# Kernel tuning notes

Hardware: AMD Instinct MI355X
Metric: run time of the kernel (lower is better)

## Reference

```python
import jax, jax.numpy as jnp
import numpy as np
from functools import partial

TOP_K = 2
LN_EPS = 1e-5


def setup_inputs() -> dict:
    key = jax.random.key(0)
    ks = jax.random.split(key, 4)
    B, T, H, F, E = 2, 2048, 1024, 4096, 8
    hidden_states = jax.random.normal(ks[0], (B, T, H), dtype=jnp.float32)
    # Router weights: original inits to zeros; use small random so routing is non-degenerate.
    router_w = jax.random.normal(ks[1], (E, H), dtype=jnp.float32) * 0.02
    router_b = jnp.zeros((E,), dtype=jnp.float32)
    W1 = jax.random.normal(ks[2], (E, H, F), dtype=jnp.float32) * (1.0 / np.sqrt(H))
    b1 = jnp.zeros((E, F), dtype=jnp.float32)
    W2 = jax.random.normal(ks[3], (E, F, H), dtype=jnp.float32) * (1.0 / np.sqrt(F))
    b2 = jnp.zeros((E, H), dtype=jnp.float32)
    ln_gamma = jnp.ones((H,), dtype=jnp.float32)
    ln_beta = jnp.zeros((H,), dtype=jnp.float32)
    return {"hidden_states": hidden_states, "router_w": router_w, "router_b": router_b,
            "W1": W1, "b1": b1, "W2": W2, "b2": b2,
            "ln_gamma": ln_gamma, "ln_beta": ln_beta}


def _layer_norm(x, gamma, beta):
    mu = jnp.mean(x, axis=-1, keepdims=True)
    var = jnp.var(x, axis=-1, keepdims=True)
    return (x - mu) * jax.lax.rsqrt(var + LN_EPS) * gamma + beta


def _moe_forward(hidden_states, router_w, router_b, W1, b1, W2, b2, ln_gamma, ln_beta):
    B, T, H = hidden_states.shape
    E = router_w.shape[0]
    N = B * T
    x = hidden_states.reshape(N, H)
    # Router (jitter=0.0, eval mode): logits [N, E]
    logits = x @ router_w.T + router_b
    topk_vals, topk_idx = jax.lax.top_k(logits, TOP_K)        # [N, K]
    topk_w = jax.nn.softmax(topk_vals, axis=-1)               # [N, K]
    # Scatter top-k weights into a dense combine matrix [N, E] (zeros elsewhere).
    probs = jnp.zeros((N, E), dtype=x.dtype).at[jnp.arange(N)[:, None], topk_idx].set(topk_w)
    # Per-expert FFN via scan over the (small, fixed) expert axis; each step is one
    # big GEMM over all tokens weighted by that expert's combine prob (0 for
    # tokens not routed to it) — same math as gather/MLP/scatter with no capacity drop.
    def body(acc, params_e):
        Wa, ba, Wb, bb, pe = params_e          # pe: [N]
        h = jax.nn.gelu(x @ Wa + ba, approximate=False)   # [N, F]
        y = h @ Wb + bb                                    # [N, H]
        return acc + y * pe[:, None], None
    out, _ = jax.lax.scan(body, jnp.zeros_like(x), (W1, b1, W2, b2, probs.T))
    out = out.reshape(B, T, H)
    return _layer_norm(out + hidden_states, ln_gamma, ln_beta)


def reference(hidden_states, router_w, router_b, W1, b1, W2, b2, ln_gamma, ln_beta):
    return _moe_forward(hidden_states, router_w, router_b, W1, b1, W2, b2, ln_gamma, ln_beta)
```

## Files before the change

kernel.cpp:

```cpp
#include <hip/hip_runtime.h>
#include <hip/hip_bf16.h>


typedef unsigned short u16;
typedef unsigned int u32;
typedef __attribute__((ext_vector_type(4))) float f32x4;
typedef __attribute__((ext_vector_type(8))) short s16x8;
typedef __attribute__((ext_vector_type(8))) unsigned short u16x8;

#define GLD16(gp, lp) __builtin_amdgcn_global_load_lds( \
    (const __attribute__((address_space(1))) void*)(gp), \
    (__attribute__((address_space(3))) void*)(lp), 16, 0, 0)

__device__ __forceinline__ u16 f2bf(float f) {
    union { float f; u32 u; } v; v.f = f;
    u32 u = v.u;
    return (u16)((u + 0x7fffu + ((u >> 16) & 1u)) >> 16);
}
__device__ __forceinline__ float bf2f(u16 h) {
    union { u32 u; float f; } v; v.u = ((u32)h) << 16; return v.f;
}

__device__ __forceinline__ float gelu_f(float v) {
    const float u = v * (0.7978845608f + 0.0356774081f * v * v);
    const float t = __expf(-2.0f * u);
    return v * __builtin_amdgcn_rcpf(1.0f + t);
}

__global__ void k_init(int* cc) { if (threadIdx.x < 16) cc[threadIdx.x] = 0; }

__device__ __forceinline__ void transp_nolds(
    const float* __restrict__ s, u16* __restrict__ d, int K, int N, int n0, int k0, int tid)
{
    const int n = n0 + tid;
    #pragma unroll 4
    for (int c8 = 0; c8 < 8; ++c8) {
        const int kb = k0 + c8 * 8;
        float v[8];
        #pragma unroll
        for (int j = 0; j < 8; ++j)
            v[j] = s[(size_t)(kb + j) * N + n];
        u16x8 o;
        #pragma unroll
        for (int j = 0; j < 8; ++j) o[j] = f2bf(v[j]);
        *(u16x8*)(d + (size_t)n * K + kb) = o;
    }
}

__global__ __launch_bounds__(256) void k_pre(
    const float* __restrict__ x, const float* __restrict__ rw, const float* __restrict__ rb,
    u16* __restrict__ xb, int* __restrict__ eidx, float* __restrict__ wgt, int* __restrict__ counts,
    const float* __restrict__ W1, u16* __restrict__ W1t)
{
    const int id = blockIdx.x;
    const int tid = threadIdx.x;

    if (id >= 1024) {
        const int id2 = id - 1024;
        const int e = id2 >> 8, rem = id2 & 255;
        const int nb = rem >> 4, kc = rem & 15;
        transp_nolds(W1 + (size_t)e * 1024 * 4096, W1t + (size_t)e * 1024 * 4096,
                     1024, 4096, nb * 256, kc * 64, tid);
        return;
    }

    const int wav = tid >> 6, lane = tid & 63;
    const int t = id * 4 + wav;
    const float* xt = x + (size_t)t * 1024;
    float acc[8] = {0.f,0.f,0.f,0.f,0.f,0.f,0.f,0.f};
    #pragma unroll
    for (int c = 0; c < 4; c++) {
        const int base = c * 256 + lane * 4;
        const float4 xv = *(const float4*)(xt + base);
        ushort4 pk;
        pk.x = f2bf(xv.x); pk.y = f2bf(xv.y); pk.z = f2bf(xv.z); pk.w = f2bf(xv.w);
        *(ushort4*)(xb + (size_t)t * 1024 + base) = pk;
        #pragma unroll
        for (int e = 0; e < 8; e++) {
            const float4 wv = *(const float4*)(rw + e * 1024 + base);
            acc[e] += xv.x * wv.x + xv.y * wv.y + xv.z * wv.z + xv.w * wv.w;
        }
    }
    #pragma unroll
    for (int e = 0; e < 8; e++) {
        #pragma unroll
        for (int s = 32; s; s >>= 1) acc[e] += __shfl_xor(acc[e], s);
    }
    if (lane == 0) {
        float v0 = -3e38f, v1 = -3e38f; int i0 = 0, i1 = 0;
        #pragma unroll
        for (int e = 0; e < 8; e++) {
            const float l = acc[e] + rb[e];
            if (l > v0) { v1 = v0; i1 = i0; v0 = l; i0 = e; }
            else if (l > v1) { v1 = l; i1 = e; }
        }
        const float w0 = 1.0f / (1.0f + expf(v1 - v0));
        eidx[2 * t] = i0; eidx[2 * t + 1] = i1;
        wgt[2 * t] = w0; wgt[2 * t + 1] = 1.0f - w0;
        atomicAdd(&counts[i0], 1); atomicAdd(&counts[i1], 1);
    }
}

__global__ __launch_bounds__(256) void k_place2(
    const int* __restrict__ eidx, const int* __restrict__ counts, int* __restrict__ cursors,
    int* __restrict__ offsets, int* __restrict__ rows, int* __restrict__ pos_of)
{
    int base[8];
    int s = 0;
    #pragma unroll
    for (int e = 0; e < 8; e++) { base[e] = s; s += counts[e]; }
    if (blockIdx.x == 0 && threadIdx.x == 0) {
        #pragma unroll
        for (int e = 0; e < 8; e++) offsets[e] = base[e];
        offsets[8] = s;
    }
    const int a = blockIdx.x * 256 + threadIdx.x;
    const int e = eidx[a];
    const int pos = base[e] + atomicAdd(&cursors[e], 1);
    rows[pos] = a >> 1;
    pos_of[a] = pos;
}

#define STAGE_T(b, k0) { \
    char* ad = (char*)At + (b) * 8192 + wav * 1024; \
    char* bd = (char*)Bt + (b) * 8192 + wav * 1024; \
    GLD16(a_src0 + (k0), ad); \
    GLD16(a_src1 + (k0), ad + 4096); \
    GLD16(b_src0 + (k0), bd); \
    GLD16(b_src1 + (k0), bd + 4096); }

#define COMPUTE_T(b) { \
    const u16* Abp = Ab + (b) * 4096; \
    const u16* Bbp = Bb + (b) * 4096; \
    s16x8 af[4], bfr[4]; \
    _Pragma("unroll") \
    for (int i = 0; i < 4; i++) { \
        af[i]  = *(const s16x8*)(Abp + i * 512); \
        bfr[i] = *(const s16x8*)(Bbp + i * 512); \
    } \
    __builtin_amdgcn_s_setprio(1); \
    _Pragma("unroll") \
    for (int mi = 0; mi < 4; mi++) \
        _Pragma("unroll") \
        for (int ni = 0; ni < 4; ni++) \
            acc[mi][ni] = __builtin_amdgcn_mfma_f32_16x16x32_bf16(af[mi], bfr[ni], acc[mi][ni], 0, 0, 0); \
    __builtin_amdgcn_s_setprio(0); }

#define VMCNT4 asm volatile("s_waitcnt vmcnt(4)" ::: "memory")
#define VMCNT0 asm volatile("s_waitcnt vmcnt(0)" ::: "memory")
#define BAR __builtin_amdgcn_s_barrier()

__global__ __launch_bounds__(256, 4) void k_gemm1f(
    const u16* __restrict__ xb, const u16* __restrict__ W1t, const float* __restrict__ b1,
    u16* __restrict__ hbuf, const int* __restrict__ rows, const int* __restrict__ offsets,
    const float* __restrict__ W2, u16* __restrict__ W2t)
{
    const int bid = blockIdx.x;
    const int tid = threadIdx.x;

    if (bid < 2048) {
        const int e = bid >> 8, rem = bid & 255;
        const int nb = rem >> 6, kc = rem & 63;
        transp_nolds(W2 + (size_t)e * 4096 * 1024, W2t + (size_t)e * 1024 * 4096,
                     4096, 1024, nb * 256, kc * 64, tid);
        return;
    }

    const int fid = bid - 2048;
    const int swz = (fid & 7) * 1024 + (fid >> 3);
    const int y = swz & 31, xx = (swz >> 5) & 31, e = swz >> 10;

    const int off = offsets[e], cnt = offsets[e + 1] - off;
    const int row0 = y * 128;
    if (row0 >= cnt) return;
    const int n0 = xx * 128;
    const int lane = tid & 63, wav = tid >> 6, lane15 = lane & 15;

    __shared__ u16 At[2][128][32];
    __shared__ u16 Bt[2][128][32];

    const int ar0 = tid >> 2;
    const int cl8 = (((tid & 3) ^ ((tid >> 3) & 3))) * 8;
    const int t0 = rows[off + min(row0 + ar0, cnt - 1)];
    const int t1 = rows[off + min(row0 + ar0 + 64, cnt - 1)];
    const u16* a_src0 = xb + (size_t)t0 * 1024 + cl8;
    const u16* a_src1 = xb + (size_t)t1 * 1024 + cl8;
    const u16* b_src0 = W1t + ((size_t)e * 4096 + n0 + ar0) * 1024 + cl8;
    const u16* b_src1 = b_src0 + (size_t)64 * 1024;

    f32x4 acc[4][4] = {};
    const int wr = wav >> 1, wc = wav & 1;
    const int koff = ((lane >> 4) ^ ((lane >> 1) & 3)) * 8;
    const u16* Ab = &At[0][wr * 64 + lane15][koff];
    const u16* Bb = &Bt[0][wc * 64 + lane15][koff];

    STAGE_T(0, 0);
    int b = 0;
    for (int k0 = 32; k0 < 1024; k0 += 32) {
        STAGE_T(b ^ 1, k0);
        VMCNT4;
        BAR;
        COMPUTE_T(b);
        BAR;
        b ^= 1;
    }
    VMCNT0;
    BAR;
    COMPUTE_T(b);

    const int rb4 = (lane >> 4) * 4;
    const int colbase = n0 + wc * 64 + lane15;
    float bias[4];
    #pragma unroll
    for (int ni = 0; ni < 4; ni++) bias[ni] = b1[e * 4096 + colbase + ni * 16];
    #pragma unroll
    for (int mi = 0; mi < 4; mi++) {
        #pragma unroll
        for (int j = 0; j < 4; j++) {
            const int lrow = wr * 64 + mi * 16 + rb4 + j;
            if (row0 + lrow < cnt) {
                const size_t gr = (size_t)(off + row0 + lrow);
                #pragma unroll
                for (int ni = 0; ni < 4; ni++) {
                    const float v = acc[mi][ni][j] + bias[ni];
                    hbuf[gr * 4096 + colbase + ni * 16] = f2bf(gelu_f(v));
                }
            }
        }
    }
}

__global__ __launch_bounds__(256, 4) void k_gemm2(
    const u16* __restrict__ hbuf, const u16* __restrict__ W2t, const float* __restrict__ b2,
    u16* __restrict__ yb, const int* __restrict__ offsets)
{
    const int fid = blockIdx.x;
    const int swz = (fid & 7) * 1024 + (fid >> 3);
    const int y = swz & 31, xx = (swz >> 5) & 7, z = swz >> 8;
    const int e = z >> 2, kq = z & 3;

    const int off = offsets[e], cnt = offsets[e + 1] - off;
    const int row0 = y * 128;
    if (row0 >= cnt) return;
    const int n0 = xx * 128;
    const int tid = threadIdx.x;
    const int lane = tid & 63, wav = tid >> 6, lane15 = lane & 15;
    const int kbase = kq * 1024;

    __shared__ u16 At[2][128][32];
    __shared__ u16 Bt[2][128][32];

    const int ar0 = tid >> 2;
    const int cl8 = (((tid & 3) ^ ((tid >> 3) & 3))) * 8;
    const u16* a_src0 = hbuf + (size_t)(off + min(row0 + ar0, cnt - 1)) * 4096 + kbase + cl8;
    const u16* a_src1 = hbuf + (size_t)(off + min(row0 + ar0 + 64, cnt - 1)) * 4096 + kbase + cl8;
    const u16* b_src0 = W2t + ((size_t)e * 1024 + n0 + ar0) * 4096 + kbase + cl8;
    const u16* b_src1 = b_src0 + (size_t)64 * 4096;

    f32x4 acc[4][4] = {};
    const int wr = wav >> 1, wc = wav & 1;
    const int koff = ((lane >> 4) ^ ((lane >> 1) & 3)) * 8;
    const u16* Ab = &At[0][wr * 64 + lane15][koff];
    const u16* Bb = &Bt[0][wc * 64 + lane15][koff];

    STAGE_T(0, 0);
    int b = 0;
    for (int k0 = 32; k0 < 1024; k0 += 32) {
        STAGE_T(b ^ 1, k0);
        VMCNT4;
        BAR;
        COMPUTE_T(b);
        BAR;
        b ^= 1;
    }
    VMCNT0;
    BAR;
    COMPUTE_T(b);

    u16* yy = yb + (size_t)kq * 8192 * 1024;
    const int rb4 = (lane >> 4) * 4;
    const int colbase = n0 + wc * 64 + lane15;
    float bias[4];
    #pragma unroll
    for (int ni = 0; ni < 4; ni++) bias[ni] = (kq == 0) ? b2[e * 1024 + colbase + ni * 16] : 0.f;
    #pragma unroll
    for (int mi = 0; mi < 4; mi++) {
        #pragma unroll
        for (int j = 0; j < 4; j++) {
            const int lrow = wr * 64 + mi * 16 + rb4 + j;
            if (row0 + lrow < cnt) {
                const size_t gr = (size_t)(off + row0 + lrow);
                #pragma unroll
                for (int ni = 0; ni < 4; ni++)
                    yy[gr * 1024 + colbase + ni * 16] = f2bf(acc[mi][ni][j] + bias[ni]);
            }
        }
    }
}

__global__ __launch_bounds__(256) void k_combine(
    const float* __restrict__ x, const u16* __restrict__ yb,
    const int* __restrict__ pos_of, const float* __restrict__ wgt,
    const float* __restrict__ gamma, const float* __restrict__ beta,
    float* __restrict__ out)
{
    const int t = blockIdx.x;
    const int tid = threadIdx.x;
    const int p0 = pos_of[2 * t], p1 = pos_of[2 * t + 1];
    const float w0 = wgt[2 * t], w1 = wgt[2 * t + 1];
    const int j4 = tid * 4;
    const float4 xv = *(const float4*)(x + (size_t)t * 1024 + j4);
    float s0[4] = {0.f, 0.f, 0.f, 0.f};
    float s1[4] = {0.f, 0.f, 0.f, 0.f};
    #pragma unroll
    for (int kq = 0; kq < 4; kq++) {
        const u16* ybq = yb + (size_t)kq * 8192 * 1024;
        const ushort4 u0 = *(const ushort4*)(ybq + (size_t)p0 * 1024 + j4);
        const ushort4 u1 = *(const ushort4*)(ybq + (size_t)p1 * 1024 + j4);
        s0[0] += bf2f(u0.x); s0[1] += bf2f(u0.y); s0[2] += bf2f(u0.z); s0[3] += bf2f(u0.w);
        s1[0] += bf2f(u1.x); s1[1] += bf2f(u1.y); s1[2] += bf2f(u1.z); s1[3] += bf2f(u1.w);
    }
    float a0 = xv.x + w0 * s0[0] + w1 * s1[0];
    float a1 = xv.y + w0 * s0[1] + w1 * s1[1];
    float a2 = xv.z + w0 * s0[2] + w1 * s1[2];
    float a3 = xv.w + w0 * s0[3] + w1 * s1[3];
    float s = a0 + a1 + a2 + a3;
    float q = a0 * a0 + a1 * a1 + a2 * a2 + a3 * a3;
    #pragma unroll
    for (int o = 32; o; o >>= 1) { s += __shfl_xor(s, o); q += __shfl_xor(q, o); }
    __shared__ float ls[4], lq[4];
    const int wav = tid >> 6, lane = tid & 63;
    if (lane == 0) { ls[wav] = s; lq[wav] = q; }
    __syncthreads();
    s = ls[0] + ls[1] + ls[2] + ls[3];
    q = lq[0] + lq[1] + lq[2] + lq[3];
    const float mu = s * (1.0f / 1024.0f);
    const float var = q * (1.0f / 1024.0f) - mu * mu;
    const float rs = rsqrtf(var + 1e-5f);
    const float4 g = *(const float4*)(gamma + j4);
    const float4 b = *(const float4*)(beta + j4);
    float4 o4;
    o4.x = (a0 - mu) * rs * g.x + b.x;
    o4.y = (a1 - mu) * rs * g.y + b.y;
    o4.z = (a2 - mu) * rs * g.z + b.z;
    o4.w = (a3 - mu) * rs * g.w + b.w;
    *(float4*)(out + (size_t)t * 1024 + j4) = o4;
}

extern "C" void kernel_launch(void* const* d_in, const int* in_sizes, int n_in,
                              void* d_out, int out_size, void* d_ws, size_t ws_size,
                              hipStream_t stream) {
    const float* x     = (const float*)d_in[0];
    const float* rw    = (const float*)d_in[1];
    const float* rb    = (const float*)d_in[2];
    const float* W1    = (const float*)d_in[3];
    const float* b1    = (const float*)d_in[4];
    const float* W2    = (const float*)d_in[5];
    const float* b2    = (const float*)d_in[6];
    const float* gamma = (const float*)d_in[7];
    const float* beta  = (const float*)d_in[8];
    float* out = (float*)d_out;

    char* p = (char*)d_ws;
    auto alloc = [&](size_t bytes) { char* r = p; p += (bytes + 255) & ~(size_t)255; return r; };
    int*   counts  = (int*)alloc(16 * sizeof(int));
    int*   cursors = counts + 8;
    int*   offsets = (int*)alloc(9 * sizeof(int));
    int*   eidx    = (int*)alloc(8192 * sizeof(int));
    float* wgt     = (float*)alloc(8192 * sizeof(float));
    int*   pos_of  = (int*)alloc(8192 * sizeof(int));
    int*   rows    = (int*)alloc(8192 * sizeof(int));
    u16*   xb      = (u16*)alloc((size_t)4096 * 1024 * 2);
    u16*   W1t     = (u16*)alloc((size_t)8 * 4096 * 1024 * 2);
    u16*   W2t     = (u16*)alloc((size_t)8 * 1024 * 4096 * 2);
    u16*   hbuf    = (u16*)alloc((size_t)8192 * 4096 * 2);
    u16* yb = W1t;

    hipLaunchKernelGGL(k_init, dim3(1), dim3(64), 0, stream, counts);
    hipLaunchKernelGGL(k_pre, dim3(3072), dim3(256), 0, stream,
                       x, rw, rb, xb, eidx, wgt, counts, W1, W1t);
    hipLaunchKernelGGL(k_place2, dim3(32), dim3(256), 0, stream,
                       eidx, counts, cursors, offsets, rows, pos_of);
    hipLaunchKernelGGL(k_gemm1f, dim3(10240), dim3(256), 0, stream,
                       xb, W1t, b1, hbuf, rows, offsets, W2, W2t);
    hipLaunchKernelGGL(k_gemm2, dim3(8192), dim3(256), 0, stream, hbuf, W2t, b2, yb, offsets);
    hipLaunchKernelGGL(k_combine, dim3(4096), dim3(256), 0, stream, x, yb, pos_of, wgt, gamma, beta, out);
}
```

Baseline: 449.4 us.

## Fuse weight fp32-to-bf16 transpose into GEMM B-tile loading

After: 475.1 us. 1.06x slower.

```diff
diff --git a/kernel.cpp b/kernel.cpp
--- a/kernel.cpp
+++ b/kernel.cpp
@@ -29,43 +29,13 @@
 
 __global__ void k_init(int* cc) { if (threadIdx.x < 16) cc[threadIdx.x] = 0; }
 
-__device__ __forceinline__ void transp_nolds(
-    const float* __restrict__ s, u16* __restrict__ d, int K, int N, int n0, int k0, int tid)
-{
-    const int n = n0 + tid;
-    #pragma unroll 4
-    for (int c8 = 0; c8 < 8; ++c8) {
-        const int kb = k0 + c8 * 8;
-        float v[8];
-        #pragma unroll
-        for (int j = 0; j < 8; ++j)
-            v[j] = s[(size_t)(kb + j) * N + n];
-        u16x8 o;
-        #pragma unroll
-        for (int j = 0; j < 8; ++j) o[j] = f2bf(v[j]);
-        *(u16x8*)(d + (size_t)n * K + kb) = o;
-    }
-}
-
-__global__ __launch_bounds__(256) void k_pre(
+__global__ __launch_bounds__(256) void k_router(
     const float* __restrict__ x, const float* __restrict__ rw, const float* __restrict__ rb,
-    u16* __restrict__ xb, int* __restrict__ eidx, float* __restrict__ wgt, int* __restrict__ counts,
-    const float* __restrict__ W1, u16* __restrict__ W1t)
-{
-    const int id = blockIdx.x;
+    u16* __restrict__ xb, int* __restrict__ eidx, float* __restrict__ wgt, int* __restrict__ counts)
+{
     const int tid = threadIdx.x;
-
-    if (id >= 1024) {
-        const int id2 = id - 1024;
-        const int e = id2 >> 8, rem = id2 & 255;
-        const int nb = rem >> 4, kc = rem & 15;
-        transp_nolds(W1 + (size_t)e * 1024 * 4096, W1t + (size_t)e * 1024 * 4096,
-                     1024, 4096, nb * 256, kc * 64, tid);
-        return;
-    }
-
     const int wav = tid >> 6, lane = tid & 63;
-    const int t = id * 4 + wav;
+    const int t = blockIdx.x * 4 + wav;
     const float* xt = x + (size_t)t * 1024;
     float acc[8] = {0.f,0.f,0.f,0.f,0.f,0.f,0.f,0.f};
     #pragma unroll
@@ -121,13 +91,10 @@
     pos_of[a] = pos;
 }
 
-#define STAGE_T(b, k0) { \
+#define STAGE_A(b, k0) { \
     char* ad = (char*)At + (b) * 8192 + wav * 1024; \
-    char* bd = (char*)Bt + (b) * 8192 + wav * 1024; \
     GLD16(a_src0 + (k0), ad); \
-    GLD16(a_src1 + (k0), ad + 4096); \
-    GLD16(b_src0 + (k0), bd); \
-    GLD16(b_src1 + (k0), bd + 4096); }
+    GLD16(a_src1 + (k0), ad + 4096); }
 
 #define COMPUTE_T(b) { \
     const u16* Abp = Ab + (b) * 4096; \
@@ -146,27 +113,14 @@
             acc[mi][ni] = __builtin_amdgcn_mfma_f32_16x16x32_bf16(af[mi], bfr[ni], acc[mi][ni], 0, 0, 0); \
     __builtin_amdgcn_s_setprio(0); }
 
-#define VMCNT4 asm volatile("s_waitcnt vmcnt(4)" ::: "memory")
 #define VMCNT0 asm volatile("s_waitcnt vmcnt(0)" ::: "memory")
 #define BAR __builtin_amdgcn_s_barrier()
 
-__global__ __launch_bounds__(256, 4) void k_gemm1f(
-    const u16* __restrict__ xb, const u16* __restrict__ W1t, const float* __restrict__ b1,
-    u16* __restrict__ hbuf, const int* __restrict__ rows, const int* __restrict__ offsets,
-    const float* __restrict__ W2, u16* __restrict__ W2t)
-{
-    const int bid = blockIdx.x;
-    const int tid = threadIdx.x;
-
-    if (bid < 2048) {
-        const int e = bid >> 8, rem = bid & 255;
-        const int nb = rem >> 6, kc = rem & 63;
-        transp_nolds(W2 + (size_t)e * 4096 * 1024, W2t + (size_t)e * 1024 * 4096,
-                     4096, 1024, nb * 256, kc * 64, tid);
-        return;
-    }
-
-    const int fid = bid - 2048;
+__global__ __launch_bounds__(256, 4) void k_gemm1(
+    const u16* __restrict__ xb, const float* __restrict__ W1, const float* __restrict__ b1,
+    u16* __restrict__ hbuf, const int* __restrict__ rows, const int* __restrict__ offsets)
+{
+    const int fid = blockIdx.x;
     const int swz = (fid & 7) * 1024 + (fid >> 3);
     const int y = swz & 31, xx = (swz >> 5) & 31, e = swz >> 10;
 
@@ -174,6 +128,7 @@
     const int row0 = y * 128;
     if (row0 >= cnt) return;
     const int n0 = xx * 128;
+    const int tid = threadIdx.x;
     const int lane = tid & 63, wav = tid >> 6, lane15 = lane & 15;
 
     __shared__ u16 At[2][128][32];
@@ -185,8 +140,29 @@
     const int t1 = rows[off + min(row0 + ar0 + 64, cnt - 1)];
     const u16* a_src0 = xb + (size_t)t0 * 1024 + cl8;
     const u16* a_src1 = xb + (size_t)t1 * 1024 + cl8;
-    const u16* b_src0 = W1t + ((size_t)e * 4096 + n0 + ar0) * 1024 + cl8;
-    const u16* b_src1 = b_src0 + (size_t)64 * 1024;
+
+    const int bn  = tid & 127;
+    const int bc0 = (tid >> 7) * 2;
+    const int bsw = (bn >> 1) & 3;
+    const float* bsrc = W1 + (size_t)e * 1024 * 4096 + n0 + bn;
+    float brg[16];
+
+    auto loadB = [&](int kk) {
+        #pragma unroll
+        for (int c = 0; c < 2; ++c)
+            #pragma unroll
+            for (int j = 0; j < 8; ++j)
+                brg[c * 8 + j] = bsrc[(size_t)(kk + (bc0 + c) * 8 + j) * 4096];
+    };
+    auto writeB = [&](int b) {
+        #pragma unroll
+        for (int c = 0; c < 2; ++c) {
+            s16x8 pk;
+            #pragma unroll
+            for (int j = 0; j < 8; ++j) pk[j] = (short)f2bf(brg[c * 8 + j]);
+            *(s16x8*)(&Bt[b][bn][((bc0 + c) ^ bsw) * 8]) = pk;
+        }
+    };
 
     f32x4 acc[4][4] = {};
     const int wr = wav >> 1, wc = wav & 1;
@@ -194,19 +170,24 @@
     const u16* Ab = &At[0][wr * 64 + lane15][koff];
     const u16* Bb = &Bt[0][wc * 64 + lane15][koff];
 
-    STAGE_T(0, 0);
-    int b = 0;
-    for (int k0 = 32; k0 < 1024; k0 += 32) {
-        STAGE_T(b ^ 1, k0);
-        VMCNT4;
-        BAR;
-        COMPUTE_T(b);
-        BAR;
-        b ^= 1;
-    }
-    VMCNT0;
-    BAR;
-    COMPUTE_T(b);
+    loadB(0);
+    STAGE_A(0, 0);
+    writeB(0);
+    VMCNT0; BAR;
+    int buf = 0;
+    for (int t = 0; t < 32; ++t) {
+        if (t < 31) {
+            loadB((t + 1) * 32);
+            STAGE_A(buf ^ 1, (t + 1) * 32);
+        }
+        COMPUTE_T(buf);
+        if (t < 31) {
+            writeB(buf ^ 1);
+            VMCNT0;
+            BAR;
+        }
+        buf ^= 1;
+    }
 
     const int rb4 = (lane >> 4) * 4;
     const int colbase = n0 + wc * 64 + lane15;
@@ -231,7 +212,7 @@
 }
 
 __global__ __launch_bounds__(256, 4) void k_gemm2(
-    const u16* __restrict__ hbuf, const u16* __restrict__ W2t, const float* __restrict__ b2,
+    const u16* __restrict__ hbuf, const float* __restrict__ W2, const float* __restrict__ b2,
     u16* __restrict__ yb, const int* __restrict__ offsets)
 {
     const int fid = blockIdx.x;
@@ -254,8 +235,29 @@
     const int cl8 = (((tid & 3) ^ ((tid >> 3) & 3))) * 8;
     const u16* a_src0 = hbuf + (size_t)(off + min(row0 + ar0, cnt - 1)) * 4096 + kbase + cl8;
     const u16* a_src1 = hbuf + (size_t)(off + min(row0 + ar0 + 64, cnt - 1)) * 4096 + kbase + cl8;
-    const u16* b_src0 = W2t + ((size_t)e * 1024 + n0 + ar0) * 4096 + kbase + cl8;
-    const u16* b_src1 = b_src0 + (size_t)64 * 4096;
+
+    const int bn  = tid & 127;
+    const int bc0 = (tid >> 7) * 2;
+    const int bsw = (bn >> 1) & 3;
+    const float* bsrc = W2 + (size_t)e * 4096 * 1024 + (size_t)kbase * 1024 + n0 + bn;
+    float brg[16];
+
+    auto loadB = [&](int kk) {
+        #pragma unroll
+        for (int c = 0; c < 2; ++c)
+            #pragma unroll
+            for (int j = 0; j < 8; ++j)
+                brg[c * 8 + j] = bsrc[(size_t)(kk + (bc0 + c) * 8 + j) * 1024];
+    };
+    auto writeB = [&](int b) {
+        #pragma unroll
+        for (int c = 0; c < 2; ++c) {
+            s16x8 pk;
+            #pragma unroll
+            for (int j = 0; j < 8; ++j) pk[j] = (short)f2bf(brg[c * 8 + j]);
+            *(s16x8*)(&Bt[b][bn][((bc0 + c) ^ bsw) * 8]) = pk;
+        }
+    };
 
     f32x4 acc[4][4] = {};
     const int wr = wav >> 1, wc = wav & 1;
@@ -263,19 +265,24 @@
     const u16* Ab = &At[0][wr * 64 + lane15][koff];
     const u16* Bb = &Bt[0][wc * 64 + lane15][koff];
 
-    STAGE_T(0, 0);
-    int b = 0;
-    for (int k0 = 32; k0 < 1024; k0 += 32) {
-        STAGE_T(b ^ 1, k0);
-        VMCNT4;
-        BAR;
-        COMPUTE_T(b);
-        BAR;
-        b ^= 1;
-    }
-    VMCNT0;
-    BAR;
-    COMPUTE_T(b);
+    loadB(0);
+    STAGE_A(0, 0);
+    writeB(0);
+    VMCNT0; BAR;
+    int buf = 0;
+    for (int t = 0; t < 32; ++t) {
+        if (t < 31) {
+            loadB((t + 1) * 32);
+            STAGE_A(buf ^ 1, (t + 1) * 32);
+        }
+        COMPUTE_T(buf);
+        if (t < 31) {
+            writeB(buf ^ 1);
+            VMCNT0;
+            BAR;
+        }
+        buf ^= 1;
+    }
 
     u16* yy = yb + (size_t)kq * 8192 * 1024;
     const int rb4 = (lane >> 4) * 4;
@@ -371,18 +378,14 @@
     int*   pos_of  = (int*)alloc(8192 * sizeof(int));
     int*   rows    = (int*)alloc(8192 * sizeof(int));
     u16*   xb      = (u16*)alloc((size_t)4096 * 1024 * 2);
-    u16*   W1t     = (u16*)alloc((size_t)8 * 4096 * 1024 * 2);
-    u16*   W2t     = (u16*)alloc((size_t)8 * 1024 * 4096 * 2);
     u16*   hbuf    = (u16*)alloc((size_t)8192 * 4096 * 2);
-    u16* yb = W1t;
+    u16*   yb      = (u16*)alloc((size_t)4 * 8192 * 1024 * 2);
 
     hipLaunchKernelGGL(k_init, dim3(1), dim3(64), 0, stream, counts);
-    hipLaunchKernelGGL(k_pre, dim3(3072), dim3(256), 0, stream,
-                       x, rw, rb, xb, eidx, wgt, counts, W1, W1t);
+    hipLaunchKernelGGL(k_router, dim3(1024), dim3(256), 0, stream, x, rw, rb, xb, eidx, wgt, counts);
     hipLaunchKernelGGL(k_place2, dim3(32), dim3(256), 0, stream,
                        eidx, counts, cursors, offsets, rows, pos_of);
-    hipLaunchKernelGGL(k_gemm1f, dim3(10240), dim3(256), 0, stream,
-                       xb, W1t, b1, hbuf, rows, offsets, W2, W2t);
-    hipLaunchKernelGGL(k_gemm2, dim3(8192), dim3(256), 0, stream, hbuf, W2t, b2, yb, offsets);
+    hipLaunchKernelGGL(k_gemm1, dim3(8192), dim3(256), 0, stream, xb, W1, b1, hbuf, rows, offsets);
+    hipLaunchKernelGGL(k_gemm2, dim3(8192), dim3(256), 0, stream, hbuf, W2, b2, yb, offsets);
     hipLaunchKernelGGL(k_combine, dim3(4096), dim3(256), 0, stream, x, yb, pos_of, wgt, gamma, beta, out);
 }
```
